# Kernel optimization log

Measured on AMD Instinct MI355X. Metric: run time of the kernel, lower is better.

The kernel has to match this reference:

```python
import jax, jax.numpy as jnp
import numpy as np

B, N, SEM, STR = 64, 512, 256, 256  # batch, tokens, sem_dim_size, str_dim_size (hidden=512)


def setup_inputs() -> dict:
    key = jax.random.key(0)
    ks = jax.random.split(key, 8)
    s = 0.02  # small init so exp(f_ij)/exp(f_i) stay well-conditioned
    return {
        "input": jax.random.normal(ks[0], (B, N, SEM + STR), jnp.float32),
        "Wp": (jax.random.normal(ks[1], (STR, STR), jnp.float32) * s),
        "bp": jnp.zeros((STR,), jnp.float32),
        "Wbil": (jax.random.normal(ks[2], (STR, STR), jnp.float32) * s),
        "bbil": jnp.zeros((), jnp.float32),
        "Wfi": (jax.random.normal(ks[3], (1, STR), jnp.float32) * s),
        "bfi": jnp.zeros((1,), jnp.float32),
        "exparam": jax.random.normal(ks[4], (1, 1, SEM), jnp.float32),
        "Wfz": (jax.random.normal(ks[5], (SEM, 2 * SEM), jnp.float32) * s),
        "bfz": jnp.zeros((SEM,), jnp.float32),
    }


def reference(input, Wp, bp, Wbil, bbil, Wfi, bfi, exparam, Wfz, bfz):
    b, n, _ = input.shape
    sem_v = input[:, :, :SEM]          # [B,N,SEM]
    str_v = input[:, :, SEM:]          # [B,N,STR]

    # NOTE: source uses tp_linear for BOTH tp and tc, and expands both with
    # unsqueeze(2), so f_ij[b,i,j] = bilinear(tp[b,i], tp[b,i]) is constant in j.
    tp = str_v @ Wp.T + bp             # [B,N,STR]
    s = jnp.einsum('bid,de,bie->bi', tp, Wbil, tp) + bbil   # [B,N]
    f_ij = jnp.broadcast_to(s[:, :, None], (b, n, n))        # [B,N,N]

    f_i = jnp.exp(str_v @ Wfi.T + bfi)[..., 0]               # [B,N]

    off = 1.0 - jnp.eye(n, dtype=input.dtype)
    A = jnp.exp(f_ij) * off                                  # zero diagonal
    deg = jnp.sum(A, axis=2)                                 # [B,N]
    L = -A + deg[:, :, None] * jnp.eye(n, dtype=input.dtype) # Laplacian
    L = L.at[:, 0, :].set(f_i)                               # root-augmented L_bar

    LLinv = jnp.linalg.inv(L)                                # [B,N,N]
    d0 = f_i * LLinv[:, :, 0]                                # root marginals [B,N]
    dg = jnp.diagonal(LLinv, axis1=-2, axis2=-1)             # [B,N]

    # tmp1 and tmp2 in the source both reduce to A[b,i,j] * diag[b,j]
    tmp = A * dg[:, None, :]
    mask1 = jnp.concatenate([jnp.zeros((n, 1)), jnp.ones((n, n - 1))], 1).astype(input.dtype)
    mask2 = jnp.concatenate([jnp.zeros((1, n)), jnp.ones((n - 1, n))], 0).astype(input.dtype)
    dx = (mask1 - mask2) * tmp                               # [B,N,N]

    d = jnp.concatenate([d0[:, None, :], dx], axis=1)        # [B,N+1,N]
    df = jnp.swapaxes(d, 1, 2)                               # [B,N,N+1]
    ssr = jnp.concatenate([jnp.broadcast_to(exparam, (b, 1, SEM)), sem_v], 1)  # [B,N+1,SEM]
    pinp = jnp.einsum('bnm,bmd->bnd', df, ssr)               # [B,N,SEM]
    # cinp = dx @ sem_v is computed in the source but never used -> omitted

    finp = jnp.concatenate([sem_v, pinp], axis=-1)           # [B,N,2*SEM]
    return jax.nn.relu(finp @ Wfz.T + bfz)                   # [B,N,SEM]
```

## Files before the change

kernel.cpp:

```cpp
#include <hip/hip_runtime.h>
#include <math.h>

#define B_    64
#define N_    512
#define SEM_  256
#define STR_  256
#define DIM_  512
#define ROWS_ (B_*N_)

#define OFF_T      0
#define OFF_QT16   65536
#define OFF_W116   98304
#define OFF_W2T    131072
#define OFF_V1     196608
#define OFF_C1     196864
#define OFF_H      197120
#define OFF_C0     197376
#define OFF_EV     197440
#define OFF_FV     230208
#define OFF_SUMP   262976
#define OFF_V2B    394048
#define OFF_ROW0   410432

typedef __bf16 bf16x8 __attribute__((ext_vector_type(8)));
typedef float  f32x4  __attribute__((ext_vector_type(4)));

__device__ __forceinline__ ushort f2b(float x) {
    return __builtin_bit_cast(ushort, (__bf16)x);
}
__device__ __forceinline__ float bflo(unsigned u) {
    return __builtin_bit_cast(float, u << 16);
}
__device__ __forceinline__ float bfhi(unsigned u) {
    return __builtin_bit_cast(float, u & 0xffff0000u);
}

__global__ __launch_bounds__(256) void k0a(
    const float* __restrict__ Wp, const float* __restrict__ bp,
    const float* __restrict__ Wbil, const float* __restrict__ Wfz,
    const float* __restrict__ exparam,
    float* __restrict__ T, ushort* __restrict__ W116, float* __restrict__ W2t,
    float* __restrict__ v1, float* __restrict__ h, float* __restrict__ c0)
{
    int t = threadIdx.x, a = blockIdx.x;
    float acc = 0.f;
    const float* wb = Wbil + a*256;
#pragma unroll 32
    for (int c = 0; c < 256; ++c) acc += wb[c] * Wp[c*256 + t];
    T[a*256 + t] = acc;
    W116[a*256 + t] = f2b(Wfz[a*512 + t]);
    W2t[t*256 + a] = Wfz[a*512 + 256 + t];
    if (a == 0) {
        float s = 0.f;
        const float* w2 = Wfz + t*512 + 256;
#pragma unroll 32
        for (int dd = 0; dd < 256; ++dd) s += w2[dd] * exparam[dd];
        v1[t] = s;
    }
    if (a == 1) {
        float g = 0.f, g2 = 0.f;
#pragma unroll 16
        for (int c = 0; c < 256; ++c) {
            g  += Wbil[t*256 + c] * bp[c];
            g2 += Wbil[c*256 + t] * bp[c];
        }
        h[t] = g + g2;
        __shared__ float red[256];
        red[t] = bp[t] * g;
        __syncthreads();
        for (int s2 = 128; s2 > 0; s2 >>= 1) {
            if (t < s2) red[t] += red[t + s2];
            __syncthreads();
        }
        if (t == 0) c0[0] = red[0];
    }
}

__global__ __launch_bounds__(256) void k0b(
    const float* __restrict__ Wp, const float* __restrict__ T,
    const float* __restrict__ h,
    ushort* __restrict__ Qt16, float* __restrict__ c1)
{
    int t = threadIdx.x, e = blockIdx.x;
    float acc = 0.f;
#pragma unroll 32
    for (int a2 = 0; a2 < 256; ++a2) acc += Wp[a2*256 + t] * T[a2*256 + e];
    Qt16[e*256 + t] = f2b(acc);
    __shared__ float red[256];
    red[t] = Wp[t*256 + e] * h[t];
    __syncthreads();
    for (int s2 = 128; s2 > 0; s2 >>= 1) {
        if (t < s2) red[t] += red[t + s2];
        __syncthreads();
    }
    if (t == 0) c1[e] = red[0];
}

__global__ __launch_bounds__(256) void k_rowstats(
    const float* __restrict__ input, const ushort* __restrict__ Qt16,
    const float* __restrict__ c1, const float* __restrict__ c0,
    const float* __restrict__ Wfi, const float* __restrict__ bbil,
    const float* __restrict__ bfi, const float* __restrict__ W2t,
    float* __restrict__ Ev, float* __restrict__ fv, float* __restrict__ v2b)
{
    __shared__ __align__(16) char smem[73728];
    ushort* Ash   = (ushort*)smem;
    ushort* Bsm0  = (ushort*)(smem + 32768);
    ushort* Bsm1  = (ushort*)(smem + 53248);
    ushort* Ush   = (ushort*)(smem + 32768);
    float*  sdiag = (float*)(smem + 65536);
    float*  fdiag = (float*)(smem + 66560);
    float*  s0sh  = (float*)(smem + 67584);
    float*  shE0  = (float*)(smem + 68608);

    int t = threadIdx.x;
    int lane = t & 63, w = t >> 6;
    int g = lane >> 4, li = lane & 15;
    long rowbase = (long)blockIdx.x * 64;
    int b = (int)(rowbase >> 9);
    int i0 = (int)(rowbase & 511);
    const float* Ab = input + rowbase*DIM_ + SEM_;
    int xs = (li & 7) << 3;
    int sn = t >> 2, sc = t & 3;

#pragma unroll
    for (int q = 0; q < 16; ++q) {
        int v = t + 256*q;
        int r = v >> 6, c4 = v & 63;
        float4 a4 = *(const float4*)(Ab + (long)r*DIM_ + c4*4);
        ushort4 b4 = make_ushort4(f2b(a4.x), f2b(a4.y), f2b(a4.z), f2b(a4.w));
        *(ushort4*)&Ash[r*256 + ((c4*4) ^ ((r & 7) << 3))] = b4;
    }
#pragma unroll
    for (int q = 0; q < 4; ++q) {
        int v = t + 256*q;
        int n = v >> 2, c = v & 3;
        *(uint4*)&Bsm0[n*40 + c*8] = *(const uint4*)&Qt16[n*256 + c*8];
    }
    __syncthreads();

    f32x4 acc[4][4];
#pragma unroll
    for (int m = 0; m < 4; ++m)
#pragma unroll
        for (int n = 0; n < 4; ++n) acc[m][n] = (f32x4){0.f, 0.f, 0.f, 0.f};

#pragma unroll
    for (int ks = 0; ks < 8; ++ks) {
        ushort* Bcur = (ks & 1) ? Bsm1 : Bsm0;
        ushort* Bnxt = (ks & 1) ? Bsm0 : Bsm1;
        int k0 = ks*32;
        uint4 breg[4];
        if (ks < 7) {
#pragma unroll
            for (int q = 0; q < 4; ++q) {
                int v = t + 256*q;
                int n = v >> 2, c = v & 3;
                breg[q] = *(const uint4*)&Qt16[n*256 + (k0 + 32) + c*8];
            }
        }
        bf16x8 af[4], bfr[4];
#pragma unroll
        for (int m = 0; m < 4; ++m)
            af[m] = *(const bf16x8*)&Ash[(m*16 + li)*256 + ((k0 + g*8) ^ xs)];
#pragma unroll
        for (int n = 0; n < 4; ++n)
            bfr[n] = *(const bf16x8*)&Bcur[(w*64 + n*16 + li)*40 + g*8];
#pragma unroll
        for (int m = 0; m < 4; ++m)
#pragma unroll
            for (int n = 0; n < 4; ++n)
                acc[m][n] = __builtin_amdgcn_mfma_f32_16x16x32_bf16(af[m], bfr[n], acc[m][n], 0, 0, 0);
        if (ks < 7) {
#pragma unroll
            for (int q = 0; q < 4; ++q) {
                int v = t + 256*q;
                int n = v >> 2, c = v & 3;
                *(uint4*)&Bnxt[n*40 + c*8] = breg[q];
            }
        }
        __syncthreads();
    }

    float c1v[4];
#pragma unroll
    for (int n = 0; n < 4; ++n) c1v[n] = c1[w*64 + n*16 + li];
#pragma unroll
    for (int m = 0; m < 4; ++m)
#pragma unroll
        for (int n = 0; n < 4; ++n)
#pragma unroll
            for (int reg = 0; reg < 4; ++reg) {
                int row = m*16 + g*4 + reg;
                int col = w*64 + n*16 + li;
                Ush[row*256 + (col ^ ((row & 7) << 3))] = f2b(acc[m][n][reg] + c1v[n]);
            }
    __syncthreads();

    f32x4 dacc[4], facc[4];
#pragma unroll
    for (int m = 0; m < 4; ++m) { dacc[m] = (f32x4){0.f,0.f,0.f,0.f}; facc[m] = (f32x4){0.f,0.f,0.f,0.f}; }
#pragma unroll
    for (int kk = 0; kk < 2; ++kk) {
        int kb = (w*2 + kk)*32 + g*8;
        float4 wf0 = *(const float4*)(Wfi + kb);
        float4 wf1 = *(const float4*)(Wfi + kb + 4);
        bf16x8 afw = (bf16x8){(__bf16)wf0.x, (__bf16)wf0.y, (__bf16)wf0.z, (__bf16)wf0.w,
                              (__bf16)wf1.x, (__bf16)wf1.y, (__bf16)wf1.z, (__bf16)wf1.w};
#pragma unroll
        for (int m = 0; m < 4; ++m) {
            int ridx = (m*16 + li)*256 + (kb ^ xs);
            bf16x8 afu = *(const bf16x8*)&Ush[ridx];
            bf16x8 bfs = *(const bf16x8*)&Ash[ridx];
            dacc[m] = __builtin_amdgcn_mfma_f32_16x16x32_bf16(afu, bfs, dacc[m], 0, 0, 0);
            facc[m] = __builtin_amdgcn_mfma_f32_16x16x32_bf16(afw, bfs, facc[m], 0, 0, 0);
        }
    }
    if (g == (li >> 2)) {
        int dr = li & 3;
#pragma unroll
        for (int m = 0; m < 4; ++m) {
            float dv = dr == 0 ? dacc[m][0] : dr == 1 ? dacc[m][1] : dr == 2 ? dacc[m][2] : dacc[m][3];
            sdiag[(m*16 + li)*4 + w] = dv;
        }
    }
    if (g == 0) {
#pragma unroll
        for (int m = 0; m < 4; ++m) fdiag[(m*16 + li)*4 + w] = facc[m][0];
    }
    __syncthreads();
    if (t < 64) {
        float ss = sdiag[t*4] + sdiag[t*4+1] + sdiag[t*4+2] + sdiag[t*4+3];
        float ff = fdiag[t*4] + fdiag[t*4+1] + fdiag[t*4+2] + fdiag[t*4+3];
        float ev = expf(ss + c0[0] + bbil[0]);
        Ev[rowbase + t] = ev;
        fv[rowbase + t] = expf(ff + bfi[0]);
        if (t == 0) shE0[0] = ev;
    }

    if (i0 == 0) {
        if (t < 64)
            *(float4*)&s0sh[t*4] = *(const float4*)(input + (long)b*512*DIM_ + t*4);
        __syncthreads();
        float a2 = 0.f;
#pragma unroll 16
        for (int d = 0; d < 256; ++d) a2 += W2t[d*256 + t] * s0sh[d];
        v2b[b*256 + t] = shE0[0] * a2;
    }
}

__global__ __launch_bounds__(256) void k_final(
    const float* __restrict__ input, const ushort* __restrict__ W116,
    const float* __restrict__ v1, const float* __restrict__ v2b,
    const float* __restrict__ Ev, const float* __restrict__ fv,
    const float* __restrict__ bfz,
    float* __restrict__ sump, float* __restrict__ row0pre,
    float* __restrict__ out)
{
    __shared__ __align__(16) char smem[74752];
    ushort* Ash    = (ushort*)smem;
    float*  Csh    = (float*)smem;
    ushort* Bsm0   = (ushort*)(smem + 32768);
    ushort* Bsm1   = (ushort*)(smem + 53248);
    float*  sumred = (float*)(smem + 40960);
    float*  cAs    = (float*)(smem + 73728);
    float*  cBs    = (float*)(smem + 73984);
    float*  EvL    = (float*)(smem + 74240);
    float*  wred   = (float*)(smem + 74496);

    int t = threadIdx.x;
    int lane = t & 63, w = t >> 6;
    int g = lane >> 4, li = lane & 15;
    long rowbase = (long)blockIdx.x * 64;
    int b = (int)(rowbase >> 9);
    int i0 = (int)(rowbase & 511);
    const float* Ab = input + rowbase*DIM_;
    int xs = (li & 7) << 3;

    float fsum = fv[b*512 + t] + fv[b*512 + 256 + t];
#pragma unroll
    for (int off = 32; off >= 1; off >>= 1) fsum += __shfl_down(fsum, off);
    if (lane == 0) wred[w] = fsum;
    __syncthreads();
    float invF = 1.0f / (wred[0] + wred[1] + wred[2] + wred[3]);

    if (t < 64) {
        int row = (int)rowbase + t;
        float fr = fv[row];
        float ev = Ev[row];
        EvL[t] = (i0 == 0 && t == 0) ? 0.f : ev;
        cAs[t] = fr * invF;
        cBs[t] = ((i0 + t) == 0) ? -invF
               : (1.0f + (fv[b*512] - fr)*invF) / (512.0f * ev);
    }

#pragma unroll
    for (int q = 0; q < 16; ++q) {
        int v = t + 256*q;
        int r = v >> 6, c4 = v & 63;
        float4 a4 = *(const float4*)(Ab + (long)r*DIM_ + c4*4);
        ushort4 b4 = make_ushort4(f2b(a4.x), f2b(a4.y), f2b(a4.z), f2b(a4.w));
        *(ushort4*)&Ash[r*256 + ((c4*4) ^ ((r & 7) << 3))] = b4;
    }
#pragma unroll
    for (int q = 0; q < 4; ++q) {
        int v = t + 256*q;
        int n = v >> 2, c = v & 3;
        *(uint4*)&Bsm0[n*40 + c*8] = *(const uint4*)&W116[n*256 + c*8];
    }
    __syncthreads();

    f32x4 acc[4][4];
#pragma unroll
    for (int m = 0; m < 4; ++m)
#pragma unroll
        for (int n = 0; n < 4; ++n) acc[m][n] = (f32x4){0.f, 0.f, 0.f, 0.f};

#pragma unroll
    for (int ks = 0; ks < 8; ++ks) {
        ushort* Bcur = (ks & 1) ? Bsm1 : Bsm0;
        ushort* Bnxt = (ks & 1) ? Bsm0 : Bsm1;
        int k0 = ks*32;
        uint4 breg[4];
        if (ks < 7) {
#pragma unroll
            for (int q = 0; q < 4; ++q) {
                int v = t + 256*q;
                int n = v >> 2, c = v & 3;
                breg[q] = *(const uint4*)&W116[n*256 + (k0 + 32) + c*8];
            }
        }
        bf16x8 af[4], bfr[4];
#pragma unroll
        for (int m = 0; m < 4; ++m)
            af[m] = *(const bf16x8*)&Ash[(m*16 + li)*256 + ((k0 + g*8) ^ xs)];
#pragma unroll
        for (int n = 0; n < 4; ++n)
            bfr[n] = *(const bf16x8*)&Bcur[(w*64 + n*16 + li)*40 + g*8];
#pragma unroll
        for (int m = 0; m < 4; ++m)
#pragma unroll
            for (int n = 0; n < 4; ++n)
                acc[m][n] = __builtin_amdgcn_mfma_f32_16x16x32_bf16(af[m], bfr[n], acc[m][n], 0, 0, 0);
        if (ks < 7) {
#pragma unroll
            for (int q = 0; q < 4; ++q) {
                int v = t + 256*q;
                int n = v >> 2, c = v & 3;
                *(uint4*)&Bnxt[n*40 + c*8] = breg[q];
            }
        }
        __syncthreads();
    }

    {
        int qq = t >> 5, c8 = t & 31;
        float p[8];
#pragma unroll
        for (int i = 0; i < 8; ++i) p[i] = 0.f;
#pragma unroll
        for (int rr = 0; rr < 8; ++rr) {
            int r = qq*8 + rr;
            float ev = EvL[r];
            uint4 uv = *(const uint4*)&Ash[r*256 + ((c8*8) ^ (rr << 3))];
            p[0] += ev * bflo(uv.x); p[1] += ev * bfhi(uv.x);
            p[2] += ev * bflo(uv.y); p[3] += ev * bfhi(uv.y);
            p[4] += ev * bflo(uv.z); p[5] += ev * bfhi(uv.z);
            p[6] += ev * bflo(uv.w); p[7] += ev * bfhi(uv.w);
        }
        *(float4*)&sumred[qq*256 + c8*8]     = (float4){p[0], p[1], p[2], p[3]};
        *(float4*)&sumred[qq*256 + c8*8 + 4] = (float4){p[4], p[5], p[6], p[7]};
    }
    __syncthreads();
    {
        float sp = 0.f;
#pragma unroll
        for (int qq = 0; qq < 8; ++qq) sp += sumred[qq*256 + t];
        sump[(long)blockIdx.x*256 + t] = sp;
    }

    float v1v[4], v2v[4], bzv[4];
#pragma unroll
    for (int n = 0; n < 4; ++n) {
        int col = w*64 + n*16 + li;
        v1v[n] = v1[col];
        v2v[n] = v2b[b*256 + col];
        bzv[n] = bfz[col];
    }

#pragma unroll
    for (int hh = 0; hh < 2; ++hh) {
        __syncthreads();
#pragma unroll
        for (int mm = 0; mm < 2; ++mm) {
            int m = hh*2 + mm;
#pragma unroll
            for (int reg = 0; reg < 4; ++reg) {
                int row = m*16 + g*4 + reg;
                float ca = cAs[row], cb = cBs[row];
                int irow = i0 + row;
#pragma unroll
                for (int n = 0; n < 4; ++n) {
                    int col = w*64 + n*16 + li;
                    float sel = (irow == 0) ? 0.f : v2v[n];
                    float val = acc[m][n][reg] + ca*v1v[n] + cb*sel + bzv[n];
                    if (irow == 0) row0pre[b*256 + col] = val;
                    Csh[(row - hh*32)*264 + col] = fmaxf(val, 0.f);
                }
            }
        }
        __syncthreads();
#pragma unroll
        for (int q = 0; q < 8; ++q) {
            int v = t + 256*q;
            int r = v >> 6, c4 = v & 63;
            *(float4*)(out + (rowbase + hh*32 + r)*256 + c4*4) = *(const float4*)&Csh[r*264 + c4*4];
        }
    }
}

__global__ __launch_bounds__(256) void k_fix(
    const float* __restrict__ sump, const float* __restrict__ fv,
    const float* __restrict__ W2t, const float* __restrict__ row0pre,
    float* __restrict__ out)
{
    int b = blockIdx.x, t = threadIdx.x;
    __shared__ float svsh[256];
    __shared__ float redF[256];
    float a = 0.f;
#pragma unroll
    for (int p = 0; p < 8; ++p) a += sump[(long)(b*8 + p)*256 + t];
    svsh[t] = a;
    redF[t] = fv[b*512 + t] + fv[b*512 + 256 + t];
    __syncthreads();
    for (int s2 = 128; s2 > 0; s2 >>= 1) {
        if (t < s2) redF[t] += redF[t + s2];
        __syncthreads();
    }
    float invF = 1.0f / redF[0];
    float a0 = 0.f;
#pragma unroll 16
    for (int d = 0; d < 256; ++d) a0 += W2t[d*256 + t] * svsh[d];
    out[((long)b*512)*256 + t] = fmaxf(row0pre[b*256 + t] - invF*a0, 0.f);
}

extern "C" void kernel_launch(void* const* d_in, const int* in_sizes, int n_in,
                              void* d_out, int out_size, void* d_ws, size_t ws_size,
                              hipStream_t stream) {
    const float* input   = (const float*)d_in[0];
    const float* Wp      = (const float*)d_in[1];
    const float* bp      = (const float*)d_in[2];
    const float* Wbil    = (const float*)d_in[3];
    const float* bbil    = (const float*)d_in[4];
    const float* Wfi     = (const float*)d_in[5];
    const float* bfi     = (const float*)d_in[6];
    const float* exparam = (const float*)d_in[7];
    const float* Wfz     = (const float*)d_in[8];
    const float* bfz     = (const float*)d_in[9];
    float* ws  = (float*)d_ws;
    float* out = (float*)d_out;

    float*  T     = ws + OFF_T;
    ushort* Qt16  = (ushort*)(ws + OFF_QT16);
    ushort* W116  = (ushort*)(ws + OFF_W116);
    float*  W2t   = ws + OFF_W2T;
    float*  v1    = ws + OFF_V1;
    float*  c1    = ws + OFF_C1;
    float*  h     = ws + OFF_H;
    float*  c0    = ws + OFF_C0;
    float*  Ev    = ws + OFF_EV;
    float*  fv    = ws + OFF_FV;
    float*  sump  = ws + OFF_SUMP;
    float*  v2b   = ws + OFF_V2B;
    float*  row0p = ws + OFF_ROW0;

    k0a<<<256, 256, 0, stream>>>(Wp, bp, Wbil, Wfz, exparam, T, W116, W2t, v1, h, c0);
    k0b<<<256, 256, 0, stream>>>(Wp, T, h, Qt16, c1);
    k_rowstats<<<ROWS_/64, 256, 0, stream>>>(input, Qt16, c1, c0, Wfi, bbil, bfi, W2t, Ev, fv, v2b);
    k_final<<<ROWS_/64, 256, 0, stream>>>(input, W116, v1, v2b, Ev, fv, bfz, sump, row0p, out);
    k_fix<<<B_, 256, 0, stream>>>(sump, fv, W2t, row0p, out);
}
```

Baseline: 84.05 us.

## Make each wave own its B-tile rows and drop per-step block barriers

The B-operand staging in the two MFMA GEMM loops is remapped so each thread loads and stores the whole 32-wide k-slice of one output column row (br = w*64+lane). Each wave then reads only the B rows it wrote itself. That removes the cross-wave dependency and lets the per-k-step __syncthreads be removed, leaving a single barrier after the loop. The cost is that each thread's global loads are now strided by 256 elements rather than coalesced across threads. The scheme also relies on intra-wave ordering, since nothing fences the LDS writes to the double buffer from earlier reads within the same wave.

```diff
diff --git a/kernel.cpp b/kernel.cpp
--- a/kernel.cpp
+++ b/kernel.cpp
@@ -121,7 +121,7 @@
     int i0 = (int)(rowbase & 511);
     const float* Ab = input + rowbase*DIM_ + SEM_;
     int xs = (li & 7) << 3;
-    int sn = t >> 2, sc = t & 3;
+    int br = w*64 + lane;
 
 #pragma unroll
     for (int q = 0; q < 16; ++q) {
@@ -132,11 +132,8 @@
         *(ushort4*)&Ash[r*256 + ((c4*4) ^ ((r & 7) << 3))] = b4;
     }
 #pragma unroll
-    for (int q = 0; q < 4; ++q) {
-        int v = t + 256*q;
-        int n = v >> 2, c = v & 3;
-        *(uint4*)&Bsm0[n*40 + c*8] = *(const uint4*)&Qt16[n*256 + c*8];
-    }
+    for (int c = 0; c < 4; ++c)
+        *(uint4*)&Bsm0[br*40 + c*8] = *(const uint4*)&Qt16[br*256 + c*8];
     __syncthreads();
 
     f32x4 acc[4][4];
@@ -153,11 +150,8 @@
         uint4 breg[4];
         if (ks < 7) {
 #pragma unroll
-            for (int q = 0; q < 4; ++q) {
-                int v = t + 256*q;
-                int n = v >> 2, c = v & 3;
-                breg[q] = *(const uint4*)&Qt16[n*256 + (k0 + 32) + c*8];
-            }
+            for (int c = 0; c < 4; ++c)
+                breg[c] = *(const uint4*)&Qt16[br*256 + (k0 + 32) + c*8];
         }
         bf16x8 af[4], bfr[4];
 #pragma unroll
@@ -173,14 +167,11 @@
                 acc[m][n] = __builtin_amdgcn_mfma_f32_16x16x32_bf16(af[m], bfr[n], acc[m][n], 0, 0, 0);
         if (ks < 7) {
 #pragma unroll
-            for (int q = 0; q < 4; ++q) {
-                int v = t + 256*q;
-                int n = v >> 2, c = v & 3;
-                *(uint4*)&Bnxt[n*40 + c*8] = breg[q];
-            }
-        }
-        __syncthreads();
-    }
+            for (int c = 0; c < 4; ++c)
+                *(uint4*)&Bnxt[br*40 + c*8] = breg[c];
+        }
+    }
+    __syncthreads();
 
     float c1v[4];
 #pragma unroll
@@ -276,6 +267,7 @@
     int i0 = (int)(rowbase & 511);
     const float* Ab = input + rowbase*DIM_;
     int xs = (li & 7) << 3;
+    int br = w*64 + lane;
 
     float fsum = fv[b*512 + t] + fv[b*512 + 256 + t];
 #pragma unroll
@@ -303,11 +295,8 @@
         *(ushort4*)&Ash[r*256 + ((c4*4) ^ ((r & 7) << 3))] = b4;
     }
 #pragma unroll
-    for (int q = 0; q < 4; ++q) {
-        int v = t + 256*q;
-        int n = v >> 2, c = v & 3;
-        *(uint4*)&Bsm0[n*40 + c*8] = *(const uint4*)&W116[n*256 + c*8];
-    }
+    for (int c = 0; c < 4; ++c)
+        *(uint4*)&Bsm0[br*40 + c*8] = *(const uint4*)&W116[br*256 + c*8];
     __syncthreads();
 
     f32x4 acc[4][4];
@@ -324,11 +313,8 @@
         uint4 breg[4];
         if (ks < 7) {
 #pragma unroll
-            for (int q = 0; q < 4; ++q) {
-                int v = t + 256*q;
-                int n = v >> 2, c = v & 3;
-                breg[q] = *(const uint4*)&W116[n*256 + (k0 + 32) + c*8];
-            }
+            for (int c = 0; c < 4; ++c)
+                breg[c] = *(const uint4*)&W116[br*256 + (k0 + 32) + c*8];
         }
         bf16x8 af[4], bfr[4];
 #pragma unroll
@@ -344,14 +330,11 @@
                 acc[m][n] = __builtin_amdgcn_mfma_f32_16x16x32_bf16(af[m], bfr[n], acc[m][n], 0, 0, 0);
         if (ks < 7) {
 #pragma unroll
-            for (int q = 0; q < 4; ++q) {
-                int v = t + 256*q;
-                int n = v >> 2, c = v & 3;
-                *(uint4*)&Bnxt[n*40 + c*8] = breg[q];
-            }
-        }
-        __syncthreads();
-    }
+            for (int c = 0; c < 4; ++c)
+                *(uint4*)&Bnxt[br*40 + c*8] = breg[c];
+        }
+    }
+    __syncthreads();
 
     {
         int qq = t >> 5, c8 = t & 31;
```

Measured after the change: 87.12 us. 3.7% more time.
